# Kernel optimization log

Measured on AMD Instinct MI355X. Metric: run time of the kernel, lower is better.

## Reference

```python
import jax, jax.numpy as jnp
import numpy as np

EPS = 1e-5
SLOPE = 0.01  # LeakyReLU default negative_slope
D_STATE = 16


def leaky(x):
    return jnp.where(x >= 0, x, SLOPE * x)


def instance_norm(x):
    # InstanceNorm3d(affine=False): normalize per (n, c) over spatial dims
    m = x.mean(axis=(2, 3, 4), keepdims=True)
    v = x.var(axis=(2, 3, 4), keepdims=True)
    return (x - m) * jax.lax.rsqrt(v + EPS)


def conv3d(x, w, b, groups=1, pad=0):
    y = jax.lax.conv_general_dilated(
        x, w, (1, 1, 1), [(pad, pad)] * 3,
        dimension_numbers=('NCDHW', 'OIDHW', 'NCDHW'),
        feature_group_count=groups)
    return y + b[None, :, None, None, None]


def conv_transpose2(x, w, b):
    # ConvTranspose3d(k=2, s=2): non-overlapping, so it is a pure einsum+interleave
    # x: [n,c,d,h,w], w: [c,o,2,2,2] (torch layout)
    y = jnp.einsum('ncdhw,coijk->nodihjwk', x, w)
    n, o, d, _, h, _, ww, _ = y.shape
    return y.reshape(n, o, 2 * d, 2 * h, 2 * ww) + b[None, :, None, None, None]


def selective_scan(u, dt, A, B, C, D):
    # u, dt: [b,l,d]; A: [d,n]; B, C: [b,l,n]; D: [d]
    dA = jnp.exp(dt[..., None] * A)                              # [b,l,d,n]
    dBu = dt[..., None] * B[:, :, None, :] * u[..., None]        # [b,l,d,n]

    def step(h, inp):
        dA_t, dBu_t, C_t = inp
        h = dA_t * h + dBu_t                                     # [b,d,n]
        y = jnp.einsum('bdn,bn->bd', h, C_t)
        return h, y

    h0 = jnp.zeros((u.shape[0],) + A.shape, u.dtype)
    _, ys = jax.lax.scan(
        step, h0,
        (dA.transpose(1, 0, 2, 3), dBu.transpose(1, 0, 2, 3), C.transpose(1, 0, 2)))
    return ys.transpose(1, 0, 2) + u * D                         # [b,l,d]


def mamba_block(x, in_proj_w, conv1d_w, conv1d_b, x_proj_w,
                dt_proj_w, dt_proj_b, A_log, D_param, out_proj_w):
    # x: [b,l,c]
    dt_rank = dt_proj_w.shape[1]
    xz = x @ in_proj_w.T                                         # [b,l,2*d_inner]
    xi, z = jnp.split(xz, 2, axis=-1)
    # causal depthwise conv1d over sequence (torch pads d_conv-1 both sides, keeps [:L])
    xi_c = xi.transpose(0, 2, 1)                                 # [b,d_inner,l]
    xi_c = jax.lax.conv_general_dilated(
        xi_c, conv1d_w, (1,), [(conv1d_w.shape[-1] - 1, 0)],
        dimension_numbers=('NCH', 'OIH', 'NCH'),
        feature_group_count=xi_c.shape[1])
    xi = jax.nn.silu(xi_c + conv1d_b[None, :, None]).transpose(0, 2, 1)  # [b,l,d_inner]
    x_dbl = xi @ x_proj_w.T
    dt, B, C = jnp.split(x_dbl, [dt_rank, dt_rank + D_STATE], axis=-1)
    dt = jax.nn.softplus(dt @ dt_proj_w.T + dt_proj_b)
    A = -jnp.exp(A_log)
    y = selective_scan(xi, dt, A, B, C, D_param)
    y = y * jax.nn.silu(z)
    return y @ out_proj_w.T


def layer_norm(x, w, b):
    m = x.mean(-1, keepdims=True)
    v = x.var(-1, keepdims=True)
    return (x - m) * jax.lax.rsqrt(v + EPS) * w + b


def up_forward(x1, x2, up_w, up_b, dc1_w, dc1_b, dc2_w, dc2_b, dc3_w, dc3_b,
               ln_w, ln_b, in_proj_w, conv1d_w, conv1d_b, x_proj_w,
               dt_proj_w, dt_proj_b, A_log, D_param, out_proj_w):
    x1 = conv_transpose2(x1, up_w, up_b)
    dZ = x2.shape[2] - x1.shape[2]
    dY = x2.shape[3] - x1.shape[3]
    dX = x2.shape[4] - x1.shape[4]
    x1 = jnp.pad(x1, ((0, 0), (0, 0),
                      (dZ // 2, dZ - dZ // 2),
                      (dY // 2, dY - dY // 2),
                      (dX // 2, dX - dX // 2)))
    x = jnp.concatenate([x2, x1], axis=1)
    # DoubleConv (residual=False since in_channels != out_channels)
    x = leaky(instance_norm(conv3d(x, dc1_w, dc1_b)))
    x = leaky(instance_norm(conv3d(x, dc2_w, dc2_b, groups=8, pad=1)))
    x = leaky(instance_norm(conv3d(x, dc3_w, dc3_b)))
    # MambaLayer over flattened spatial tokens
    b, c, d, h, w = x.shape
    t = x.transpose(0, 2, 3, 4, 1).reshape(b, d * h * w, c)
    t = layer_norm(t, ln_w, ln_b)
    t = mamba_block(t, in_proj_w, conv1d_w, conv1d_b, x_proj_w,
                    dt_proj_w, dt_proj_b, A_log, D_param, out_proj_w)
    return t.reshape(b, d, h, w, c).transpose(0, 4, 1, 2, 3)


def setup_inputs() -> dict:
    key = jax.random.key(0)
    ks = jax.random.split(key, 20)
    c_out = 32      # out_channels / d_model
    d_inner = 64    # expand * d_model
    dt_rank = 2     # ceil(32/16)
    s = 0.02
    return {
        'x1': jax.random.normal(ks[0], (2, 32, 8, 16, 16), jnp.float32),
        'x2': jax.random.normal(ks[1], (2, 32, 16, 32, 32), jnp.float32),
        'up_w': jax.random.normal(ks[2], (32, 32, 2, 2, 2), jnp.float32) * s,
        'up_b': jnp.zeros((32,), jnp.float32),
        'dc1_w': jax.random.normal(ks[3], (32, 64, 1, 1, 1), jnp.float32) * s,
        'dc1_b': jnp.zeros((32,), jnp.float32),
        'dc2_w': jax.random.normal(ks[4], (32, 4, 3, 3, 3), jnp.float32) * s,
        'dc2_b': jnp.zeros((32,), jnp.float32),
        'dc3_w': jax.random.normal(ks[5], (32, 32, 1, 1, 1), jnp.float32) * s,
        'dc3_b': jnp.zeros((32,), jnp.float32),
        'ln_w': jnp.ones((c_out,), jnp.float32),
        'ln_b': jnp.zeros((c_out,), jnp.float32),
        'in_proj_w': jax.random.normal(ks[6], (2 * d_inner, c_out), jnp.float32) * s,
        'conv1d_w': jax.random.normal(ks[7], (d_inner, 1, 4), jnp.float32) * s,
        'conv1d_b': jnp.zeros((d_inner,), jnp.float32),
        'x_proj_w': jax.random.normal(ks[8], (dt_rank + 2 * D_STATE, d_inner), jnp.float32) * s,
        'dt_proj_w': jax.random.normal(ks[9], (d_inner, dt_rank), jnp.float32) * s,
        'dt_proj_b': jnp.full((d_inner,), -4.0, jnp.float32),
        'A_log': jnp.log(jnp.tile(jnp.arange(1.0, D_STATE + 1.0, dtype=jnp.float32), (d_inner, 1))),
        'D_param': jnp.ones((d_inner,), jnp.float32),
        'out_proj_w': jax.random.normal(ks[10], (c_out, d_inner), jnp.float32) * s,
    }


def reference(x1, x2, up_w, up_b, dc1_w, dc1_b, dc2_w, dc2_b, dc3_w, dc3_b,
              ln_w, ln_b, in_proj_w, conv1d_w, conv1d_b, x_proj_w,
              dt_proj_w, dt_proj_b, A_log, D_param, out_proj_w):
    return up_forward(x1, x2, up_w, up_b, dc1_w, dc1_b, dc2_w, dc2_b, dc3_w, dc3_b,
                      ln_w, ln_b, in_proj_w, conv1d_w, conv1d_b, x_proj_w,
                      dt_proj_w, dt_proj_b, A_log, D_param, out_proj_w)
```

## Files before the change

kernel.cpp:

```cpp
#include <hip/hip_runtime.h>

#define TPB 256
#define S_TOT 16384
#define NCHUNK 256
#define EPS 1e-5f
#define SLOPE 0.01f

__device__ __forceinline__ float leakyf(float v){ return v > 0.f ? v : SLOPE * v; }
__device__ __forceinline__ float siluf(float v){ return v / (1.f + __expf(-v)); }

__global__ __launch_bounds__(TPB) void k_upc1(
    const float* __restrict__ x1, const float* __restrict__ x2,
    const float* __restrict__ upw, const float* __restrict__ upb,
    const float* __restrict__ w1, const float* __restrict__ b1,
    float* __restrict__ c1, float* st1p) {
  __shared__ float wq[8192];
  __shared__ float sup[64*33];
  __shared__ float red[4][8][2];
  int t = threadIdx.x, bid = blockIdx.x;
  int sb = bid & 255, n = bid >> 8;
  int p = t & 63, os = t >> 6;
  int s = sb*64 + p;
  for (int i = t; i < 8192; i += TPB) wq[i] = upw[i];
  __syncthreads();
  int z = s >> 10, y = (s >> 5) & 31, x = s & 31;
  int tap = ((z & 1)*2 + (y & 1))*2 + (x & 1);
  int xb = n*65536 + (z >> 1)*256 + (y >> 1)*16 + (x >> 1);
  float xv[32];
  #pragma unroll
  for (int c = 0; c < 32; c++) xv[c] = x1[xb + c*2048];
  float up[8];
  #pragma unroll
  for (int j = 0; j < 8; j++) up[j] = upb[os*8 + j];
  #pragma unroll
  for (int c = 0; c < 32; c++) {
    #pragma unroll
    for (int j = 0; j < 8; j++)
      up[j] += xv[c] * wq[c*256 + (os*8 + j)*8 + tap];
  }
  #pragma unroll
  for (int j = 0; j < 8; j++) sup[p*33 + os*8 + j] = up[j];
  __syncthreads();
  int c0 = os*8;
  float acc[8];
  #pragma unroll
  for (int j = 0; j < 8; j++) acc[j] = b1[c0 + j];
  const float* px2 = x2 + n*32*S_TOT + s;
  #pragma unroll
  for (int i = 0; i < 32; i++) {
    float v = px2[i*S_TOT];
    #pragma unroll
    for (int j = 0; j < 8; j++) acc[j] += v * w1[(c0 + j)*64 + i];
  }
  #pragma unroll
  for (int o = 0; o < 32; o++) {
    float v = sup[p*33 + o];
    #pragma unroll
    for (int j = 0; j < 8; j++) acc[j] += v * w1[(c0 + j)*64 + 32 + o];
  }
  #pragma unroll
  for (int j = 0; j < 8; j++)
    c1[(n*32 + c0 + j)*S_TOT + s] = acc[j];
  int wv = t >> 6;
  #pragma unroll
  for (int j = 0; j < 8; j++) {
    float sm = acc[j], sq = acc[j]*acc[j];
    #pragma unroll
    for (int o = 32; o > 0; o >>= 1) { sm += __shfl_down(sm, o); sq += __shfl_down(sq, o); }
    if ((t & 63) == 0) { red[wv][j][0] = sm; red[wv][j][1] = sq; }
  }
  __syncthreads();
  if (t < 64) {
    int w2 = t >> 4, j = (t >> 1) & 7, m = t & 1;
    st1p[((n*32 + w2*8 + j)*2 + m)*256 + sb] = red[w2][j][m];
  }
}

__global__ __launch_bounds__(TPB) void k_conv2(
    const float* __restrict__ c1, const float* __restrict__ w,
    const float* __restrict__ bias, const float* st1p,
    float* __restrict__ c2, float* st2p) {
  __shared__ float ws[432];
  __shared__ float smom[4][2];
  __shared__ float mrs[4][2];
  __shared__ float red[4][4][2];
  int bid = blockIdx.x, t = threadIdx.x;
  int sb = bid & 63, g = (bid >> 6) & 7, n = bid >> 9;
  int s = (sb << 8) + t;
  for (int i = t; i < 432; i += TPB) ws[i] = w[(g*4)*108 + i];
  {
    int pp = t >> 5, l = t & 31;
    if (pp < 8) {
      int j = pp & 3, m = pp >> 2;
      const float* sp = st1p + ((n*32 + g*4 + j)*2 + m)*256;
      float v = 0.f;
      #pragma unroll
      for (int k = 0; k < 8; k++) v += sp[l + 32*k];
      v += __shfl_down(v, 16); v += __shfl_down(v, 8); v += __shfl_down(v, 4);
      v += __shfl_down(v, 2);  v += __shfl_down(v, 1);
      if (l == 0) smom[j][m] = v;
    }
  }
  __syncthreads();
  if (t < 4) {
    float m = smom[t][0] * (1.f/S_TOT);
    mrs[t][0] = m; mrs[t][1] = rsqrtf(smom[t][1]*(1.f/S_TOT) - m*m + EPS);
  }
  __syncthreads();
  int z = s >> 10, y = (s >> 5) & 31, x = s & 31;
  float mx0 = (x > 0) ? 1.f : 0.f, mx2 = (x < 31) ? 1.f : 0.f;
  float acc[4];
  #pragma unroll
  for (int oc = 0; oc < 4; oc++) acc[oc] = bias[g*4 + oc];
  const float* pbase = c1 + (n*32 + g*4)*S_TOT;
  #pragma unroll
  for (int ic = 0; ic < 4; ic++) {
    const float* pc = pbase + ic*S_TOT;
    float m = mrs[ic][0], rs = mrs[ic][1];
    #pragma unroll
    for (int dz = 0; dz < 3; dz++) {
      int zz = z + dz - 1;
      int zc = zz < 0 ? 0 : (zz > 15 ? 15 : zz);
      float vz = (zz >= 0 && zz < 16) ? 1.f : 0.f;
      #pragma unroll
      for (int dy = 0; dy < 3; dy++) {
        int yy = y + dy - 1;
        int yc = yy < 0 ? 0 : (yy > 31 ? 31 : yy);
        float vzy = vz * ((yy >= 0 && yy < 32) ? 1.f : 0.f);
        const float* pr = pc + zc*1024 + yc*32 + x;
        float p0 = leakyf((pr[-1] - m)*rs) * (vzy*mx0);
        float p1 = leakyf((pr[ 0] - m)*rs) * vzy;
        float p2 = leakyf((pr[ 1] - m)*rs) * (vzy*mx2);
        int wb = ic*27 + dz*9 + dy*3;
        #pragma unroll
        for (int oc = 0; oc < 4; oc++) {
          const float* wo = &ws[oc*108 + wb];
          acc[oc] += p0*wo[0] + p1*wo[1] + p2*wo[2];
        }
      }
    }
  }
  float sm[4], sq[4];
  #pragma unroll
  for (int oc = 0; oc < 4; oc++) {
    c2[(n*32 + g*4 + oc)*S_TOT + s] = acc[oc];
    sm[oc] = acc[oc]; sq[oc] = acc[oc]*acc[oc];
  }
  #pragma unroll
  for (int o = 32; o > 0; o >>= 1) {
    #pragma unroll
    for (int oc = 0; oc < 4; oc++) {
      sm[oc] += __shfl_down(sm[oc], o);
      sq[oc] += __shfl_down(sq[oc], o);
    }
  }
  int lane = t & 63, wv = t >> 6;
  if (lane == 0) {
    #pragma unroll
    for (int oc = 0; oc < 4; oc++) { red[wv][oc][0] = sm[oc]; red[wv][oc][1] = sq[oc]; }
  }
  __syncthreads();
  if (t < 8) {
    int oc = t & 3, m = t >> 2;
    float a = red[0][oc][m] + red[1][oc][m] + red[2][oc][m] + red[3][oc][m];
    st2p[((n*32 + g*4 + oc)*2 + m)*64 + sb] = a;
  }
}

__global__ __launch_bounds__(TPB) void k_conv3(
    const float* __restrict__ c2, const float* __restrict__ w,
    const float* __restrict__ bias, const float* st2p,
    float* __restrict__ c3, float* st3p) {
  __shared__ float ws[256];
  __shared__ float ssum[32][2];
  __shared__ float mrs[32][2];
  __shared__ float red[4][8][2];
  int t = threadIdx.x;
  int idx = blockIdx.x * TPB + t;
  int s = idx & 16383;
  int n = (idx >> 14) & 1;
  int q = idx >> 15;
  int sb = blockIdx.x & 63;
  int c0 = q*8;
  if (t < 256) ws[t] = w[c0*32 + t];
  if (t < 64) {
    int c = t >> 1, m = t & 1;
    const float* sp = st2p + ((n*32 + c)*2 + m)*64;
    float v = 0.f;
    #pragma unroll
    for (int k = 0; k < 64; k++) v += sp[k];
    ssum[c][m] = v;
  }
  __syncthreads();
  if (t < 32) {
    float m = ssum[t][0] * (1.f/S_TOT);
    mrs[t][0] = m; mrs[t][1] = rsqrtf(ssum[t][1]*(1.f/S_TOT) - m*m + EPS);
  }
  __syncthreads();
  const float* pin = c2 + n*32*S_TOT + s;
  float acc[8];
  #pragma unroll
  for (int j = 0; j < 8; j++) acc[j] = bias[c0 + j];
  #pragma unroll
  for (int i = 0; i < 32; i++) {
    float v = leakyf((pin[i*S_TOT] - mrs[i][0]) * mrs[i][1]);
    #pragma unroll
    for (int j = 0; j < 8; j++) acc[j] += v * ws[j*32 + i];
  }
  #pragma unroll
  for (int j = 0; j < 8; j++)
    c3[(n*32 + c0 + j)*S_TOT + s] = acc[j];
  int wv = t >> 6;
  #pragma unroll
  for (int j = 0; j < 8; j++) {
    float sm = acc[j], sq = acc[j]*acc[j];
    #pragma unroll
    for (int o = 32; o > 0; o >>= 1) { sm += __shfl_down(sm, o); sq += __shfl_down(sq, o); }
    if ((t & 63) == 0) { red[wv][j][0] = sm; red[wv][j][1] = sq; }
  }
  __syncthreads();
  if (t < 16) {
    int j = t >> 1, m = t & 1;
    float a = red[0][j][m] + red[1][j][m] + red[2][j][m] + red[3][j][m];
    st3p[((n*32 + c0 + j)*2 + m)*64 + sb] = a;
  }
}

__global__ __launch_bounds__(TPB) void k_token(
    const float* __restrict__ c3, const float* st3p,
    const float* __restrict__ lnw, const float* __restrict__ lnb,
    const float* __restrict__ ipw, const float* __restrict__ c1w,
    const float* __restrict__ c1b, const float* __restrict__ xpw,
    const float* __restrict__ dtw, const float* __restrict__ dtbi,
    float* __restrict__ zb, float* __restrict__ u, float* __restrict__ dt,
    float* __restrict__ Bb, float* __restrict__ Cc) {
  __shared__ float un[4224];
  __shared__ float xpf[2210];
  __shared__ float sxi[1216];
  __shared__ float lnwb[64];
  __shared__ float mrs[64];
  __shared__ float ssum[64];
  float* Wraw = un;
  float* tk   = un;
  float* mv   = un + 684;
  float* su2  = un;
  float* xd   = un + 1040;

  int t = threadIdx.x, bid = blockIdx.x;
  int tok0 = bid * 16;
  int n = tok0 >> 14, s0 = tok0 & 16383;

  if (t < 64) {
    int c = t >> 1, m = t & 1;
    const float* sp = st3p + ((n*32 + c)*2 + m)*64;
    float v = 0.f;
    #pragma unroll
    for (int k = 0; k < 64; k++) v += sp[k];
    ssum[c*2 + m] = v;
  }
  for (int i = t; i < 4096; i += TPB) {
    int f = i >> 5, c = i & 31;
    Wraw[f*33 + c] = ipw[i];
  }
  for (int i = t; i < 2176; i += TPB) {
    int f = i >> 6, dd = i & 63;
    xpf[f*65 + dd] = xpw[i];
  }
  if (t < 32) { lnwb[t] = lnw[t]; lnwb[32 + t] = lnb[t]; }
  __syncthreads();
  if (t < 32) {
    float m = ssum[t*2] * (1.f/S_TOT);
    mrs[t*2] = m; mrs[t*2 + 1] = rsqrtf(ssum[t*2 + 1]*(1.f/S_TOT) - m*m + EPS);
  }
  int fr = t & 127, half = t >> 7;
  float wreg[32];
  float S1 = 0.f, S2 = 0.f;
  #pragma unroll
  for (int c = 0; c < 32; c++) {
    float wa = Wraw[fr*33 + c];
    wreg[c] = wa * lnwb[c];
    S1 += wreg[c];
    S2 += wa * lnwb[32 + c];
  }
  __syncthreads();
  for (int i = t; i < 608; i += TPB) {
    int c = i / 19, lt = i - c*19;
    int sg = s0 - 3 + lt;
    int sgc = sg < 0 ? 0 : sg;
    float raw = c3[(n*32 + c)*S_TOT + sgc];
    tk[lt*36 + c] = leakyf((raw - mrs[c*2]) * mrs[c*2 + 1]);
  }
  __syncthreads();
  if (t < 19) {
    float mean = 0.f;
    #pragma unroll
    for (int c = 0; c < 32; c++) mean += tk[t*36 + c];
    mean *= (1.f/32.f);
    float var = 0.f;
    #pragma unroll
    for (int c = 0; c < 32; c++) { float d2 = tk[t*36 + c] - mean; var += d2*d2; }
    mv[t*2] = mean; mv[t*2 + 1] = rsqrtf(var*(1.f/32.f) + EPS);
  }
  __syncthreads();
  for (int lt = half; lt < 19; lt += 2) {
    float acc = 0.f;
    #pragma unroll
    for (int c4 = 0; c4 < 8; c4++) {
      float4 tq = *(const float4*)(tk + lt*36 + 4*c4);
      acc += wreg[4*c4]*tq.x + wreg[4*c4+1]*tq.y + wreg[4*c4+2]*tq.z + wreg[4*c4+3]*tq.w;
    }
    float mean = mv[lt*2], rst = mv[lt*2 + 1];
    float r = rst*(acc - mean*S1) + S2;
    int sg = s0 - 3 + lt;
    if (fr < 64) {
      sxi[lt*64 + fr] = (sg < 0) ? 0.f : r;
    } else if (lt >= 3) {
      zb[(tok0 + lt - 3)*64 + (fr - 64)] = r;
    }
  }
  __syncthreads();
  int ch = t & 63;
  {
    float cw0 = c1w[ch*4], cw1 = c1w[ch*4+1], cw2 = c1w[ch*4+2], cw3 = c1w[ch*4+3];
    float cb = c1b[ch];
    #pragma unroll
    for (int r = 0; r < 4; r++) {
      int lt = (t >> 6) + 4*r;
      float acc = cb + sxi[lt*64 + ch]*cw0 + sxi[(lt+1)*64 + ch]*cw1
                     + sxi[(lt+2)*64 + ch]*cw2 + sxi[(lt+3)*64 + ch]*cw3;
      float uv = siluf(acc);
      u[(tok0 + lt)*64 + ch] = uv;
      su2[lt*65 + ch] = uv;
    }
  }
  __syncthreads();
  for (int i = t; i < 544; i += TPB) {
    int lt = i / 34, f = i - lt*34;
    float a = 0.f;
    #pragma unroll
    for (int dd = 0; dd < 64; dd++) a += xpf[f*65 + dd] * su2[lt*65 + dd];
    xd[lt*34 + f] = a;
  }
  __syncthreads();
  {
    float dw0 = dtw[ch*2], dw1 = dtw[ch*2+1], db = dtbi[ch];
    #pragma unroll
    for (int r = 0; r < 4; r++) {
      int lt = (t >> 6) + 4*r;
      int token = tok0 + lt;
      float dv = xd[lt*34]*dw0 + xd[lt*34 + 1]*dw1 + db;
      dt[token*64 + ch] = fmaxf(dv, 0.f) + log1pf(__expf(-fabsf(dv)));
      if (ch < 16)      Bb[token*16 + ch]      = xd[lt*34 + 2 + ch];
      else if (ch < 32) Cc[token*16 + ch - 16] = xd[lt*34 + 2 + ch];
    }
  }
}


__global__ __launch_bounds__(TPB) void k_scan1(
    const float* __restrict__ dt, const float* __restrict__ u,
    const float* __restrict__ Bb, const float* __restrict__ Alog,
    float* __restrict__ cA, float* __restrict__ cX) {
  __shared__ __align__(16) float sdt[1024], su[1024], sB[256];
  int bid = blockIdx.x, t = threadIdx.x;
  int chunk = bid & 255, b = bid >> 8;
  int q = t & 3, d = t >> 2;
  float Ar[4];
  #pragma unroll
  for (int j = 0; j < 4; j++) Ar[j] = -__expf(Alog[d*16 + 4*q + j]);
  float h[4] = {0.f,0.f,0.f,0.f};
  float sdts = 0.f;
  int tg0 = b*S_TOT + chunk*64;
  for (int tile = 0; tile < 4; tile++) {
    int base = tg0 + tile*16;
    for (int i = t; i < 1024; i += TPB) { sdt[i] = dt[base*64 + i]; su[i] = u[base*64 + i]; }
    sB[t] = Bb[base*16 + t];
    __syncthreads();
    #pragma unroll
    for (int tt = 0; tt < 16; tt++) {
      float dtv = sdt[tt*64 + d], uv = su[tt*64 + d];
      sdts += dtv;
      float du = dtv * uv;
      float4 Bq = *(const float4*)(sB + tt*16 + q*4);
      h[0] = __expf(Ar[0]*dtv)*h[0] + Bq.x*du;
      h[1] = __expf(Ar[1]*dtv)*h[1] + Bq.y*du;
      h[2] = __expf(Ar[2]*dtv)*h[2] + Bq.z*du;
      h[3] = __expf(Ar[3]*dtv)*h[3] + Bq.w*du;
    }
    __syncthreads();
  }
  #pragma unroll
  for (int j = 0; j < 4; j++) {
    int idx = (((b*64 + d)*16 + 4*q + j)*NCHUNK) + chunk;
    cA[idx] = __expf(Ar[j]*sdts);
    cX[idx] = h[j];
  }
}

__global__ __launch_bounds__(TPB) void k_scan2(
    const float* __restrict__ cA, float* __restrict__ cX) {
  int t = threadIdx.x;
  int w = blockIdx.x*4 + (t >> 6);
  int lane = t & 63;
  int b = w >> 10, d = (w >> 4) & 63, nn = w & 15;
  int base = ((b*64 + d)*16 + nn)*NCHUNK;
  float4 a = *(const float4*)(cA + base + lane*4);
  float4 x = *(const float4*)(cX + base + lane*4);
  float A = a.x*a.y*a.z*a.w;
  float X = ((x.x*a.y + x.y)*a.z + x.z)*a.w + x.w;
  #pragma unroll
  for (int off = 1; off < 64; off <<= 1) {
    float Ap = __shfl_up(A, off);
    float Xp = __shfl_up(X, off);
    if (lane >= off) { X = A*Xp + X; A = A*Ap; }
  }
  float Xe = __shfl_up(X, 1);
  if (lane == 0) Xe = 0.f;
  float r = Xe;
  float4 o;
  o.x = r; r = a.x*r + x.x;
  o.y = r; r = a.y*r + x.y;
  o.z = r; r = a.z*r + x.z;
  o.w = r;
  *(float4*)(cX + base + lane*4) = o;
}

__global__ __launch_bounds__(TPB) void k_scan3(
    const float* __restrict__ dt, const float* __restrict__ u,
    const float* __restrict__ Bb, const float* __restrict__ Cc,
    const float* __restrict__ Alog, const float* __restrict__ Dp,
    const float* __restrict__ zb, const float* __restrict__ cX,
    const float* __restrict__ opw, float* __restrict__ out) {
  __shared__ __align__(16) float sdt[1024], su[1024], sB[256], sC[256];
  __shared__ float gt[64*65];
  int bid = blockIdx.x, t = threadIdx.x;
  int chunk = bid & 255, b = bid >> 8;
  int q = t & 3, d = t >> 2;
  float Ar[4];
  #pragma unroll
  for (int j = 0; j < 4; j++) Ar[j] = -__expf(Alog[d*16 + 4*q + j]);
  float h[4];
  #pragma unroll
  for (int j = 0; j < 4; j++)
    h[j] = cX[(((b*64 + d)*16 + 4*q + j)*NCHUNK) + chunk];
  float Dv = Dp[d];
  int tg0 = b*S_TOT + chunk*64;
  for (int tile = 0; tile < 4; tile++) {
    int base = tg0 + tile*16;
    for (int i = t; i < 1024; i += TPB) {
      sdt[i] = dt[base*64 + i];
      su[i]  = u[base*64 + i];
      gt[(tile*16 + (i >> 6))*65 + (i & 63)] = zb[base*64 + i];
    }
    sB[t] = Bb[base*16 + t];
    sC[t] = Cc[base*16 + t];
    __syncthreads();
    #pragma unroll
    for (int tt = 0; tt < 16; tt++) {
      float dtv = sdt[tt*64 + d], uv = su[tt*64 + d];
      float du = dtv * uv;
      float4 Bq = *(const float4*)(sB + tt*16 + q*4);
      float4 Cq = *(const float4*)(sC + tt*16 + q*4);
      h[0] = __expf(Ar[0]*dtv)*h[0] + Bq.x*du;
      h[1] = __expf(Ar[1]*dtv)*h[1] + Bq.y*du;
      h[2] = __expf(Ar[2]*dtv)*h[2] + Bq.z*du;
      h[3] = __expf(Ar[3]*dtv)*h[3] + Bq.w*du;
      float yp = h[0]*Cq.x + h[1]*Cq.y + h[2]*Cq.z + h[3]*Cq.w;
      yp += __shfl_xor(yp, 1);
      yp += __shfl_xor(yp, 2);
      if (q == 0) {
        float zv = gt[(tile*16 + tt)*65 + d];
        gt[(tile*16 + tt)*65 + d] = (yp + uv*Dv) * siluf(zv);
      }
    }
    __syncthreads();
  }
  {
    int sl = t & 63, cb = t >> 6;
    float acc[8] = {0.f,0.f,0.f,0.f,0.f,0.f,0.f,0.f};
    const float* wp = opw + cb*8*64;
    #pragma unroll
    for (int dd = 0; dd < 64; dd++) {
      float v = gt[sl*65 + dd];
      #pragma unroll
      for (int j = 0; j < 8; j++) acc[j] += v * wp[j*64 + dd];
    }
    #pragma unroll
    for (int j = 0; j < 8; j++)
      out[(b*32 + cb*8 + j)*S_TOT + chunk*64 + sl] = acc[j];
  }
}

extern "C" void kernel_launch(void* const* d_in, const int* in_sizes, int n_in,
                              void* d_out, int out_size, void* d_ws, size_t ws_size,
                              hipStream_t stream) {
  const float* x1    = (const float*)d_in[0];
  const float* x2    = (const float*)d_in[1];
  const float* upw   = (const float*)d_in[2];
  const float* upb   = (const float*)d_in[3];
  const float* dc1w  = (const float*)d_in[4];
  const float* dc1b  = (const float*)d_in[5];
  const float* dc2w  = (const float*)d_in[6];
  const float* dc2b  = (const float*)d_in[7];
  const float* dc3w  = (const float*)d_in[8];
  const float* dc3b  = (const float*)d_in[9];
  const float* lnw   = (const float*)d_in[10];
  const float* lnb   = (const float*)d_in[11];
  const float* ipw   = (const float*)d_in[12];
  const float* c1w   = (const float*)d_in[13];
  const float* c1b   = (const float*)d_in[14];
  const float* xpw   = (const float*)d_in[15];
  const float* dtw   = (const float*)d_in[16];
  const float* dtbi  = (const float*)d_in[17];
  const float* Alog  = (const float*)d_in[18];
  const float* Dp    = (const float*)d_in[19];
  const float* opw   = (const float*)d_in[20];
  float* out = (float*)d_out;

  float* ws = (float*)d_ws;
  float* st1p  = ws + 0;
  float* st2p  = ws + 32768;
  float* st3p  = ws + 40960;
  float* c1    = ws + 49152;
  float* c2    = ws + 1097728;
  float* c3    = ws + 2146304;
  float* zb    = ws + 3194880;
  float* ub    = ws + 5292032;
  float* dtb   = ws + 7389184;
  float* Bb    = ws + 9486336;
  float* Cc    = ws + 10010624;
  float* cA    = ws + 10534912;
  float* cX    = ws + 11059200;

  k_upc1 <<<512,  TPB, 0, stream>>>(x1, x2, upw, upb, dc1w, dc1b, c1, st1p);
  k_conv2<<<1024, TPB, 0, stream>>>(c1, dc2w, dc2b, st1p, c2, st2p);
  k_conv3<<<512,  TPB, 0, stream>>>(c2, dc3w, dc3b, st2p, c3, st3p);
  k_token<<<2048, TPB, 0, stream>>>(c3, st3p, lnw, lnb, ipw, c1w, c1b, xpw,
                                    dtw, dtbi, zb, ub, dtb, Bb, Cc);
  k_scan1<<<512,  TPB, 0, stream>>>(dtb, ub, Bb, Alog, cA, cX);
  k_scan2<<<512,  TPB, 0, stream>>>(cA, cX);
  k_scan3<<<512,  TPB, 0, stream>>>(dtb, ub, Bb, Cc, Alog, Dp, zb, cX, opw, out);
}
```

Measured before the change: 244.8 us.

## Stage normalized conv2 halo in shared memory and vectorize token/scan loads

k_conv2 now loads a normalized, LeakyReLU-applied halo tile of the input into shared memory once per block, so each input is not re-normalized 27 times per output and bounds checks leave the inner loop. k_token reads in_proj weights straight from global as float4 instead of staging them in shared memory, and the x_proj matvec is rewritten with float4 shared loads, each thread computing three features. The scan kernels load dt and u with float4. Shared memory use grows in conv2, which may lower occupancy.

```diff
diff --git a/kernel.cpp b/kernel.cpp
--- a/kernel.cpp
+++ b/kernel.cpp
@@ -81,13 +81,15 @@
     const float* __restrict__ bias, const float* st1p,
     float* __restrict__ c2, float* st2p) {
   __shared__ float ws[432];
+  __shared__ float tile[4080];
   __shared__ float smom[4][2];
   __shared__ float mrs[4][2];
   __shared__ float red[4][4][2];
   int bid = blockIdx.x, t = threadIdx.x;
   int sb = bid & 63, g = (bid >> 6) & 7, n = bid >> 9;
-  int s = (sb << 8) + t;
-  for (int i = t; i < 432; i += TPB) ws[i] = w[(g*4)*108 + i];
+  int s0 = sb << 8;
+  int z = s0 >> 10, y0 = (s0 >> 5) & 31;
+  for (int i = t; i < 432; i += TPB) ws[i] = w[g*432 + i];
   {
     int pp = t >> 5, l = t & 31;
     if (pp < 8) {
@@ -107,30 +109,31 @@
     mrs[t][0] = m; mrs[t][1] = rsqrtf(smom[t][1]*(1.f/S_TOT) - m*m + EPS);
   }
   __syncthreads();
-  int z = s >> 10, y = (s >> 5) & 31, x = s & 31;
-  float mx0 = (x > 0) ? 1.f : 0.f, mx2 = (x < 31) ? 1.f : 0.f;
+  const float* cbase = c1 + (n*32 + g*4)*S_TOT;
+  for (int i = t; i < 4080; i += TPB) {
+    int ic = i / 1020, r = i - ic*1020;
+    int zo = r / 340, r2 = r - zo*340;
+    int yo = r2 / 34, xo = r2 - yo*34;
+    int zz = z + zo - 1, yy = y0 + yo - 1, xx = xo - 1;
+    float v = 0.f;
+    if (zz >= 0 && zz < 16 && yy >= 0 && yy < 32 && xx >= 0 && xx < 32)
+      v = leakyf((cbase[ic*S_TOT + zz*1024 + yy*32 + xx] - mrs[ic][0]) * mrs[ic][1]);
+    tile[i] = v;
+  }
+  __syncthreads();
+  int ty = t >> 5, x = t & 31;
+  int s = s0 + t;
   float acc[4];
   #pragma unroll
   for (int oc = 0; oc < 4; oc++) acc[oc] = bias[g*4 + oc];
-  const float* pbase = c1 + (n*32 + g*4)*S_TOT;
   #pragma unroll
   for (int ic = 0; ic < 4; ic++) {
-    const float* pc = pbase + ic*S_TOT;
-    float m = mrs[ic][0], rs = mrs[ic][1];
     #pragma unroll
     for (int dz = 0; dz < 3; dz++) {
-      int zz = z + dz - 1;
-      int zc = zz < 0 ? 0 : (zz > 15 ? 15 : zz);
-      float vz = (zz >= 0 && zz < 16) ? 1.f : 0.f;
       #pragma unroll
       for (int dy = 0; dy < 3; dy++) {
-        int yy = y + dy - 1;
-        int yc = yy < 0 ? 0 : (yy > 31 ? 31 : yy);
-        float vzy = vz * ((yy >= 0 && yy < 32) ? 1.f : 0.f);
-        const float* pr = pc + zc*1024 + yc*32 + x;
-        float p0 = leakyf((pr[-1] - m)*rs) * (vzy*mx0);
-        float p1 = leakyf((pr[ 0] - m)*rs) * vzy;
-        float p2 = leakyf((pr[ 1] - m)*rs) * (vzy*mx2);
+        const float* tr = tile + ((ic*3 + dz)*10 + ty + dy)*34 + x;
+        float p0 = tr[0], p1 = tr[1], p2 = tr[2];
         int wb = ic*27 + dz*9 + dy*3;
         #pragma unroll
         for (int oc = 0; oc < 4; oc++) {
@@ -234,17 +237,16 @@
     const float* __restrict__ dtw, const float* __restrict__ dtbi,
     float* __restrict__ zb, float* __restrict__ u, float* __restrict__ dt,
     float* __restrict__ Bb, float* __restrict__ Cc) {
-  __shared__ float un[4224];
-  __shared__ float xpf[2210];
+  __shared__ float un[1632];
+  __shared__ float xpf[3264];
   __shared__ float sxi[1216];
   __shared__ float lnwb[64];
   __shared__ float mrs[64];
   __shared__ float ssum[64];
-  float* Wraw = un;
-  float* tk   = un;
-  float* mv   = un + 684;
-  float* su2  = un;
-  float* xd   = un + 1040;
+  float* tk  = un;
+  float* mv  = un + 684;
+  float* su2 = un;
+  float* xd  = un + 1088;
 
   int t = threadIdx.x, bid = blockIdx.x;
   int tok0 = bid * 16;
@@ -258,13 +260,9 @@
     for (int k = 0; k < 64; k++) v += sp[k];
     ssum[c*2 + m] = v;
   }
-  for (int i = t; i < 4096; i += TPB) {
-    int f = i >> 5, c = i & 31;
-    Wraw[f*33 + c] = ipw[i];
-  }
-  for (int i = t; i < 2176; i += TPB) {
-    int f = i >> 6, dd = i & 63;
-    xpf[f*65 + dd] = xpw[i];
+  for (int i = t; i < 3264; i += TPB) {
+    int f = i / 68, dd = i - f*68;
+    xpf[i] = (f < 34 && dd < 64) ? xpw[f*64 + dd] : 0.f;
   }
   if (t < 32) { lnwb[t] = lnw[t]; lnwb[32 + t] = lnb[t]; }
   __syncthreads();
@@ -275,12 +273,18 @@
   int fr = t & 127, half = t >> 7;
   float wreg[32];
   float S1 = 0.f, S2 = 0.f;
-  #pragma unroll
-  for (int c = 0; c < 32; c++) {
-    float wa = Wraw[fr*33 + c];
-    wreg[c] = wa * lnwb[c];
-    S1 += wreg[c];
-    S2 += wa * lnwb[32 + c];
+  {
+    const float4* wp = (const float4*)(ipw + fr*32);
+    #pragma unroll
+    for (int c4 = 0; c4 < 8; c4++) {
+      float4 w4 = wp[c4];
+      float l0 = lnwb[4*c4], l1 = lnwb[4*c4+1], l2 = lnwb[4*c4+2], l3 = lnwb[4*c4+3];
+      float b0 = lnwb[32+4*c4], b1 = lnwb[33+4*c4], b2 = lnwb[34+4*c4], b3 = lnwb[35+4*c4];
+      S2 += w4.x*b0 + w4.y*b1 + w4.z*b2 + w4.w*b3;
+      wreg[4*c4]   = w4.x*l0; wreg[4*c4+1] = w4.y*l1;
+      wreg[4*c4+2] = w4.z*l2; wreg[4*c4+3] = w4.w*l3;
+      S1 += wreg[4*c4] + wreg[4*c4+1] + wreg[4*c4+2] + wreg[4*c4+3];
+    }
   }
   __syncthreads();
   for (int i = t; i < 608; i += TPB) {
@@ -330,16 +334,31 @@
                      + sxi[(lt+2)*64 + ch]*cw2 + sxi[(lt+3)*64 + ch]*cw3;
       float uv = siluf(acc);
       u[(tok0 + lt)*64 + ch] = uv;
-      su2[lt*65 + ch] = uv;
-    }
-  }
-  __syncthreads();
-  for (int i = t; i < 544; i += TPB) {
-    int lt = i / 34, f = i - lt*34;
-    float a = 0.f;
-    #pragma unroll
-    for (int dd = 0; dd < 64; dd++) a += xpf[f*65 + dd] * su2[lt*65 + dd];
-    xd[lt*34 + f] = a;
+      su2[lt*68 + ch] = uv;
+    }
+  }
+  __syncthreads();
+  {
+    int lt = t >> 4, fg = t & 15;
+    int f0 = fg*3;
+    const float* sr = su2 + lt*68;
+    const float* xr0 = xpf + f0*68;
+    const float* xr1 = xpf + (f0+1)*68;
+    const float* xr2 = xpf + (f0+2)*68;
+    float a0 = 0.f, a1 = 0.f, a2 = 0.f;
+    #pragma unroll
+    for (int c4 = 0; c4 < 16; c4++) {
+      float4 uq = *(const float4*)(sr + 4*c4);
+      float4 q0 = *(const float4*)(xr0 + 4*c4);
+      float4 q1 = *(const float4*)(xr1 + 4*c4);
+      float4 q2 = *(const float4*)(xr2 + 4*c4);
+      a0 += uq.x*q0.x + uq.y*q0.y + uq.z*q0.z + uq.w*q0.w;
+      a1 += uq.x*q1.x + uq.y*q1.y + uq.z*q1.z + uq.w*q1.w;
+      a2 += uq.x*q2.x + uq.y*q2.y + uq.z*q2.z + uq.w*q2.w;
+    }
+    if (f0     < 34) xd[lt*34 + f0]     = a0;
+    if (f0 + 1 < 34) xd[lt*34 + f0 + 1] = a1;
+    if (f0 + 2 < 34) xd[lt*34 + f0 + 2] = a2;
   }
   __syncthreads();
   {
@@ -373,7 +392,11 @@
   int tg0 = b*S_TOT + chunk*64;
   for (int tile = 0; tile < 4; tile++) {
     int base = tg0 + tile*16;
-    for (int i = t; i < 1024; i += TPB) { sdt[i] = dt[base*64 + i]; su[i] = u[base*64 + i]; }
+    {
+      int i = t*4;
+      *(float4*)(sdt + i) = *(const float4*)(dt + base*64 + i);
+      *(float4*)(su  + i) = *(const float4*)(u  + base*64 + i);
+    }
     sB[t] = Bb[base*16 + t];
     __syncthreads();
     #pragma unroll
@@ -447,11 +470,13 @@
   int tg0 = b*S_TOT + chunk*64;
   for (int tile = 0; tile < 4; tile++) {
     int base = tg0 + tile*16;
-    for (int i = t; i < 1024; i += TPB) {
-      sdt[i] = dt[base*64 + i];
-      su[i]  = u[base*64 + i];
+    {
+      int i = t*4;
+      *(float4*)(sdt + i) = *(const float4*)(dt + base*64 + i);
+      *(float4*)(su  + i) = *(const float4*)(u  + base*64 + i);
+    }
+    for (int i = t; i < 1024; i += TPB)
       gt[(tile*16 + (i >> 6))*65 + (i & 63)] = zb[base*64 + i];
-    }
     sB[t] = Bb[base*16 + t];
     sC[t] = Cc[base*16 + t];
     __syncthreads();
```

New measurement: 248.5 us. Within noise of the previous version (+1.5%).
